# Kernel tuning notes

Measured on AMD Instinct MI355X. Metric: run time of the kernel, lower is better.

Reference implementation:

```python
import jax, jax.numpy as jnp
import numpy as np

B, T, C = 2, 2048, 768
H = 12
D = C // H
HID = 4 * C
EPS = 1e-5
LS_INIT = 1e-4


def _ln(x, g, b):
    mu = jnp.mean(x, axis=-1, keepdims=True)
    var = jnp.mean((x - mu) ** 2, axis=-1, keepdims=True)
    return (x - mu) * jax.lax.rsqrt(var + EPS) * g + b


def setup_inputs() -> dict:
    key = jax.random.key(0)
    ks = jax.random.split(key, 10)
    s = lambda fan_in: 1.0 / np.sqrt(fan_in)
    return {
        "x": jax.random.normal(ks[0], (B, T, C), dtype=jnp.float32),
        "mask_logits": jnp.zeros((B, 1, T, T), dtype=jnp.float32),
        "bias": jax.random.normal(ks[1], (B, H, T, T), dtype=jnp.float32),
        "ln1_g": jnp.ones((C,), jnp.float32),
        "ln1_b": jnp.zeros((C,), jnp.float32),
        "qkv_w": jax.random.normal(ks[2], (3 * C, C), jnp.float32) * s(C),
        "qkv_b": jnp.zeros((3 * C,), jnp.float32),
        "proj_w": jax.random.normal(ks[3], (C, C), jnp.float32) * s(C),
        "proj_b": jnp.zeros((C,), jnp.float32),
        "ls1": jnp.full((C,), LS_INIT, jnp.float32),
        "ln2_g": jnp.ones((C,), jnp.float32),
        "ln2_b": jnp.zeros((C,), jnp.float32),
        "w1": jax.random.normal(ks[4], (HID, C), jnp.float32) * s(C),
        "b1": jnp.zeros((HID,), jnp.float32),
        "w2": jax.random.normal(ks[5], (C, HID), jnp.float32) * s(HID),
        "b2": jnp.zeros((C,), jnp.float32),
        "ls2": jnp.full((C,), LS_INIT, jnp.float32),
    }


def reference(x, mask_logits, bias, ln1_g, ln1_b, qkv_w, qkv_b, proj_w, proj_b,
              ls1, ln2_g, ln2_b, w1, b1, w2, b2, ls2):
    scale = 1.0 / np.sqrt(D)
    xn = _ln(x, ln1_g, ln1_b)
    qkv = xn @ qkv_w.T + qkv_b                      # [B,T,3C]
    qkv = qkv.reshape(B, T, 3, H, D).transpose(2, 0, 3, 1, 4)  # [3,B,H,T,D]
    q, k, v = qkv[0], qkv[1], qkv[2]
    logits = jnp.einsum('bhqd,bhkd->bhqk', q, k) * scale + bias + mask_logits
    attn = jax.nn.softmax(logits, axis=-1)          # [B,H,T,T]
    y = jnp.einsum('bhqk,bhkd->bhqd', attn, v)      # [B,H,T,D]
    y = y.transpose(0, 2, 1, 3).reshape(B, T, C)
    y = y @ proj_w.T + proj_b
    x = x + y * ls1
    h = _ln(x, ln2_g, ln2_b)
    h = jax.nn.gelu(h @ w1.T + b1, approximate=False)
    h = h @ w2.T + b2
    x = x + h * ls2
    return x, jax.lax.stop_gradient(attn)
```

## Files before the change

### kernel.cpp

```cpp
#include <hip/hip_runtime.h>
#include <hip/hip_bf16.h>
#include <math.h>

#define B_ 2
#define T_ 2048
#define C_ 768
#define H_ 12
#define D_ 64
#define HID_ 3072
#define NROW 4096
#define N3C 2304

typedef short bf16x8 __attribute__((ext_vector_type(8)));
typedef float f32x4 __attribute__((ext_vector_type(4)));
typedef unsigned short u16;
typedef unsigned int u32;

__device__ inline u16 f2bf(float f) {
    u32 u = __float_as_uint(f);
    u32 r = (u + 0x7fffu + ((u >> 16) & 1u)) >> 16;
    return (u16)r;
}

__global__ __launch_bounds__(256) void cvt_bf16_kernel(const float* __restrict__ s,
                                                       u16* __restrict__ d, int n) {
    int i = (blockIdx.x * 256 + threadIdx.x) * 4;
    if (i >= n) return;
    float4 v = *(const float4*)(s + i);
    ushort4 o;
    o.x = f2bf(v.x); o.y = f2bf(v.y); o.z = f2bf(v.z); o.w = f2bf(v.w);
    *(ushort4*)(d + i) = o;
}

__global__ __launch_bounds__(256) void ln_kernel(const float* __restrict__ x,
                                                 const float* __restrict__ g,
                                                 const float* __restrict__ b,
                                                 u16* __restrict__ out) {
    int row = blockIdx.x, t = threadIdx.x;
    const float* xr = x + (size_t)row * C_;
    float v[3], s = 0.f, sq = 0.f;
#pragma unroll
    for (int i = 0; i < 3; i++) {
        v[i] = xr[i * 256 + t];
        s += v[i]; sq += v[i] * v[i];
    }
    for (int m = 32; m; m >>= 1) { s += __shfl_xor(s, m); sq += __shfl_xor(sq, m); }
    __shared__ float ss[4], ssq[4];
    int wid = t >> 6;
    if ((t & 63) == 0) { ss[wid] = s; ssq[wid] = sq; }
    __syncthreads();
    s = ss[0] + ss[1] + ss[2] + ss[3];
    sq = ssq[0] + ssq[1] + ssq[2] + ssq[3];
    float mu = s * (1.f / C_);
    float var = sq * (1.f / C_) - mu * mu;
    float rstd = rsqrtf(var + 1e-5f);
#pragma unroll
    for (int i = 0; i < 3; i++) {
        int c = i * 256 + t;
        out[(size_t)row * C_ + c] = f2bf((v[i] - mu) * rstd * g[c] + b[c]);
    }
}

template <int EPI>
__global__ __launch_bounds__(256) void gemm_kernel(const u16* __restrict__ A,
                                                   const u16* __restrict__ W,
                                                   const float* __restrict__ bias,
                                                   float* __restrict__ outf,
                                                   u16* __restrict__ outb,
                                                   const float* __restrict__ res,
                                                   const float* __restrict__ ls,
                                                   int N, int K) {
    __shared__ u16 Alds[128 * 64];
    __shared__ u16 Blds[128 * 64];
    int tid = threadIdx.x;
    int m0 = blockIdx.y * 128, n0 = blockIdx.x * 128;
    int lane = tid & 63, wid = tid >> 6;
    int wr = wid >> 1, wc = wid & 1;
    int lr = lane & 15, lq = lane >> 4;

    f32x4 acc[4][4];
#pragma unroll
    for (int i = 0; i < 4; i++)
#pragma unroll
        for (int j = 0; j < 4; j++) acc[i][j] = (f32x4){0.f, 0.f, 0.f, 0.f};

    int nk = K >> 6;
    const u16* Ab = A + (size_t)m0 * K;
    const u16* Wb = W + (size_t)n0 * K;
    bf16x8 ra[4], rb[4];
#pragma unroll
    for (int i = 0; i < 4; i++) {
        int c = tid + i * 256, row = c >> 3, j = c & 7;
        ra[i] = *(const bf16x8*)(Ab + (size_t)row * K + j * 8);
        rb[i] = *(const bf16x8*)(Wb + (size_t)row * K + j * 8);
    }
    for (int kt = 0; kt < nk; ++kt) {
        __syncthreads();
#pragma unroll
        for (int i = 0; i < 4; i++) {
            int c = tid + i * 256, row = c >> 3, j = c & 7;
            int off = row * 64 + ((j ^ (row & 7)) << 3);
            *(bf16x8*)(Alds + off) = ra[i];
            *(bf16x8*)(Blds + off) = rb[i];
        }
        __syncthreads();
        if (kt + 1 < nk) {
            int k0 = (kt + 1) << 6;
#pragma unroll
            for (int i = 0; i < 4; i++) {
                int c = tid + i * 256, row = c >> 3, j = c & 7;
                ra[i] = *(const bf16x8*)(Ab + (size_t)row * K + k0 + j * 8);
                rb[i] = *(const bf16x8*)(Wb + (size_t)row * K + k0 + j * 8);
            }
        }
#pragma unroll
        for (int s = 0; s < 2; s++) {
            bf16x8 af[4], bw[4];
#pragma unroll
            for (int i = 0; i < 4; i++) {
                int arow = wr * 64 + i * 16 + lr;
                af[i] = *(const bf16x8*)(Alds + arow * 64 + (((4 * s + lq) ^ (arow & 7)) << 3));
                int brow = wc * 64 + i * 16 + lr;
                bw[i] = *(const bf16x8*)(Blds + brow * 64 + (((4 * s + lq) ^ (brow & 7)) << 3));
            }
#pragma unroll
            for (int i = 0; i < 4; i++)
#pragma unroll
                for (int j = 0; j < 4; j++)
                    acc[i][j] = __builtin_amdgcn_mfma_f32_16x16x32_bf16(af[i], bw[j], acc[i][j], 0, 0, 0);
        }
    }
#pragma unroll
    for (int i = 0; i < 4; i++) {
#pragma unroll
        for (int j = 0; j < 4; j++) {
#pragma unroll
            for (int r = 0; r < 4; r++) {
                int gm = m0 + wr * 64 + i * 16 + lq * 4 + r;
                int gn = n0 + wc * 64 + j * 16 + lr;
                float val = acc[i][j][r] + bias[gn];
                if (EPI == 0) {
                    outb[(size_t)gm * N + gn] = f2bf(val);
                } else if (EPI == 1) {
                    float gl = 0.5f * val * (1.f + erff(val * 0.70710678118654752f));
                    outb[(size_t)gm * N + gn] = f2bf(gl);
                } else {
                    outf[(size_t)gm * N + gn] = res[(size_t)gm * N + gn] + ls[gn] * val;
                }
            }
        }
    }
}

__global__ __launch_bounds__(256) void vtrans_kernel(const u16* __restrict__ qkv,
                                                     u16* __restrict__ vt) {
    __shared__ u16 tile[64 * 72];
    int t0 = blockIdx.x * 64, h = blockIdx.y, b = blockIdx.z;
    int tid = threadIdx.x;
#pragma unroll
    for (int i = 0; i < 2; i++) {
        int c = tid + i * 256, tr = c >> 3, j = c & 7;
        bf16x8 v = *(const bf16x8*)(qkv + (size_t)(b * T_ + t0 + tr) * N3C + 1536 + h * 64 + j * 8);
        *(bf16x8*)(tile + tr * 72 + j * 8) = v;
    }
    __syncthreads();
#pragma unroll
    for (int i = 0; i < 2; i++) {
        int c = tid + i * 256, d = c >> 3, tj = c & 7;
        bf16x8 o;
#pragma unroll
        for (int k = 0; k < 8; k++) o[k] = (short)tile[(tj * 8 + k) * 72 + d];
        *(bf16x8*)(vt + (size_t)((b * H_ + h) * 64 + d) * T_ + t0 + tj * 8) = o;
    }
}

__global__ __launch_bounds__(256, 2) void attn_kernel(const u16* __restrict__ qkv,
                                                      const u16* __restrict__ vt,
                                                      const float* __restrict__ bias,
                                                      const float* __restrict__ mask,
                                                      float* __restrict__ attn_out,
                                                      u16* __restrict__ ybuf) {
    __shared__ u16 S[16 * 2048];
    __shared__ float rinv_lds[16];
    char* Sb = (char*)S;
    int qt = blockIdx.x, h = blockIdx.y, b = blockIdx.z;
    int tid = threadIdx.x, lane = tid & 63, wid = tid >> 6;
    int lr = lane & 15, lq = lane >> 4;
    int q0 = qt * 16;
    size_t bh = (size_t)(b * H_ + h);
    const float scale = 0.125f;

    const u16* qp = qkv + (size_t)(b * T_ + q0 + lr) * N3C + h * 64;
    bf16x8 qa0 = *(const bf16x8*)(qp + lq * 8);
    bf16x8 qa1 = *(const bf16x8*)(qp + 32 + lq * 8);
    const u16* kbase = qkv + (size_t)(b * T_ + wid * 512 + lr) * N3C + 768 + h * 64 + lq * 8;
#pragma unroll 4
    for (int ct = 0; ct < 32; ++ct) {
        bf16x8 kf0 = *(const bf16x8*)(kbase + (size_t)ct * 16 * N3C);
        bf16x8 kf1 = *(const bf16x8*)(kbase + (size_t)ct * 16 * N3C + 32);
        f32x4 a = (f32x4){0.f, 0.f, 0.f, 0.f};
        a = __builtin_amdgcn_mfma_f32_16x16x32_bf16(kf0, qa0, a, 0, 0, 0);
        a = __builtin_amdgcn_mfma_f32_16x16x32_bf16(kf1, qa1, a, 0, 0, 0);
        int colbase = wid * 512 + ct * 16;
        ushort4 pk;
        pk.x = f2bf(a[0] * scale);
        pk.y = f2bf(a[1] * scale);
        pk.z = f2bf(a[2] * scale);
        pk.w = f2bf(a[3] * scale);
        *(ushort4*)(Sb + (((u32)lr * 4096 + 2 * colbase + 8 * lq) ^ ((lr & 7) << 4))) = pk;
    }
    __syncthreads();

    const float* bb = bias + (bh * T_ + q0 + wid * 4) * T_;
    const float* mb = mask + ((size_t)b * T_ + q0 + wid * 4) * T_;
    float lsum4[4] = {0.f, 0.f, 0.f, 0.f};
#pragma unroll
    for (int ch = 0; ch < 8; ++ch) {
        int col = ch * 256 + lane * 4;
        float4 b4[4], m4[4];
#pragma unroll
        for (int rr = 0; rr < 4; ++rr) {
            b4[rr] = *(const float4*)(bb + (size_t)rr * T_ + col);
            m4[rr] = *(const float4*)(mb + (size_t)rr * T_ + col);
        }
#pragma unroll
        for (int rr = 0; rr < 4; ++rr) {
            int r = wid * 4 + rr;
            u32 addr = ((u32)r * 4096 + (u32)col * 2) ^ ((u32)(r & 7) << 4);
            uint2 s2 = *(const uint2*)(Sb + addr);
            float e0 = __expf(__uint_as_float(s2.x << 16) + b4[rr].x + m4[rr].x);
            float e1 = __expf(__uint_as_float(s2.x & 0xffff0000u) + b4[rr].y + m4[rr].y);
            float e2 = __expf(__uint_as_float(s2.y << 16) + b4[rr].z + m4[rr].z);
            float e3 = __expf(__uint_as_float(s2.y & 0xffff0000u) + b4[rr].w + m4[rr].w);
            lsum4[rr] += (e0 + e1) + (e2 + e3);
            uint2 o;
            o.x = ((u32)f2bf(e1) << 16) | (u32)f2bf(e0);
            o.y = ((u32)f2bf(e3) << 16) | (u32)f2bf(e2);
            *(uint2*)(Sb + addr) = o;
        }
    }
    float rinv_r[4];
#pragma unroll
    for (int rr = 0; rr < 4; ++rr) {
        float ls = lsum4[rr];
        for (int m = 32; m; m >>= 1) ls += __shfl_xor(ls, m);
        rinv_r[rr] = 1.f / ls;
        if (lane == 0) rinv_lds[wid * 4 + rr] = rinv_r[rr];
    }
    __syncthreads();

    float* ao_base = attn_out + (bh * T_ + q0 + wid * 4) * T_;
#pragma unroll
    for (int ch = 0; ch < 8; ++ch) {
        int col = ch * 256 + lane * 4;
#pragma unroll
        for (int rr = 0; rr < 4; ++rr) {
            int r = wid * 4 + rr;
            u32 addr = ((u32)r * 4096 + (u32)col * 2) ^ ((u32)(r & 7) << 4);
            uint2 s2 = *(const uint2*)(Sb + addr);
            float rv = rinv_r[rr];
            float4 o;
            o.x = __uint_as_float(s2.x << 16) * rv;
            o.y = __uint_as_float(s2.x & 0xffff0000u) * rv;
            o.z = __uint_as_float(s2.y << 16) * rv;
            o.w = __uint_as_float(s2.y & 0xffff0000u) * rv;
            *(float4*)(ao_base + (size_t)rr * T_ + col) = o;
        }
    }

    f32x4 acc = (f32x4){0.f, 0.f, 0.f, 0.f};
    const u16* vtp = vt + (bh * 64 + wid * 16 + lr) * (size_t)T_ + lq * 8;
#pragma unroll 4
    for (int ks = 0; ks < 64; ++ks) {
        bf16x8 pf = *(const bf16x8*)(Sb + (((u32)lr * 4096 + ks * 64 + lq * 16) ^ ((lr & 7) << 4)));
        bf16x8 vf = *(const bf16x8*)(vtp + ks * 32);
        acc = __builtin_amdgcn_mfma_f32_16x16x32_bf16(pf, vf, acc, 0, 0, 0);
    }
#pragma unroll
    for (int r = 0; r < 4; r++) {
        int row = lq * 4 + r;
        float y = acc[r] * rinv_lds[row];
        ybuf[(size_t)(b * T_ + q0 + row) * C_ + h * 64 + wid * 16 + lr] = f2bf(y);
    }
}

extern "C" void kernel_launch(void* const* d_in, const int* in_sizes, int n_in,
                              void* d_out, int out_size, void* d_ws, size_t ws_size,
                              hipStream_t stream) {
    const float* x = (const float*)d_in[0];
    const float* mask = (const float*)d_in[1];
    const float* bias = (const float*)d_in[2];
    const float* ln1g = (const float*)d_in[3];
    const float* ln1b = (const float*)d_in[4];
    const float* qkvw = (const float*)d_in[5];
    const float* qkvb = (const float*)d_in[6];
    const float* projw = (const float*)d_in[7];
    const float* projb = (const float*)d_in[8];
    const float* ls1 = (const float*)d_in[9];
    const float* ln2g = (const float*)d_in[10];
    const float* ln2b = (const float*)d_in[11];
    const float* w1 = (const float*)d_in[12];
    const float* b1 = (const float*)d_in[13];
    const float* w2 = (const float*)d_in[14];
    const float* b2 = (const float*)d_in[15];
    const float* ls2 = (const float*)d_in[16];

    char* ws = (char*)d_ws;
    size_t off = 0;
    u16* qkvw_b = (u16*)(ws + off); off += (size_t)N3C * C_ * 2;
    u16* projw_b = (u16*)(ws + off); off += (size_t)C_ * C_ * 2;
    u16* w1_b = (u16*)(ws + off); off += (size_t)HID_ * C_ * 2;
    u16* w2_b = (u16*)(ws + off); off += (size_t)C_ * HID_ * 2;
    u16* xn = (u16*)(ws + off); off += (size_t)NROW * C_ * 2;
    u16* qkvbuf = (u16*)(ws + off); off += (size_t)NROW * N3C * 2;
    u16* vt = (u16*)(ws + off); off += (size_t)B_ * H_ * D_ * T_ * 2;
    u16* g = qkvbuf;
    u16* ybuf = (u16*)(ws + off); off += (size_t)NROW * C_ * 2;
    float* x1 = (float*)(ws + off); off += (size_t)NROW * C_ * 4;
    (void)ws_size; (void)n_in; (void)in_sizes; (void)out_size;

    float* outx = (float*)d_out;
    float* attn_out = outx + (size_t)NROW * C_;

    cvt_bf16_kernel<<<(N3C * C_ / 4 + 255) / 256, 256, 0, stream>>>(qkvw, qkvw_b, N3C * C_);
    cvt_bf16_kernel<<<(C_ * C_ / 4 + 255) / 256, 256, 0, stream>>>(projw, projw_b, C_ * C_);
    cvt_bf16_kernel<<<(HID_ * C_ / 4 + 255) / 256, 256, 0, stream>>>(w1, w1_b, HID_ * C_);
    cvt_bf16_kernel<<<(C_ * HID_ / 4 + 255) / 256, 256, 0, stream>>>(w2, w2_b, C_ * HID_);

    ln_kernel<<<NROW, 256, 0, stream>>>(x, ln1g, ln1b, xn);
    gemm_kernel<0><<<dim3(N3C / 128, NROW / 128), 256, 0, stream>>>(
        xn, qkvw_b, qkvb, nullptr, qkvbuf, nullptr, nullptr, N3C, C_);
    vtrans_kernel<<<dim3(T_ / 64, H_, B_), 256, 0, stream>>>(qkvbuf, vt);
    attn_kernel<<<dim3(T_ / 16, H_, B_), 256, 0, stream>>>(qkvbuf, vt, bias, mask, attn_out, ybuf);
    gemm_kernel<2><<<dim3(C_ / 128, NROW / 128), 256, 0, stream>>>(
        ybuf, projw_b, projb, x1, nullptr, x, ls1, C_, C_);
    ln_kernel<<<NROW, 256, 0, stream>>>(x1, ln2g, ln2b, xn);
    gemm_kernel<1><<<dim3(HID_ / 128, NROW / 128), 256, 0, stream>>>(
        xn, w1_b, b1, nullptr, g, nullptr, nullptr, HID_, C_);
    gemm_kernel<2><<<dim3(C_ / 128, NROW / 128), 256, 0, stream>>>(
        g, w2_b, b2, outx, nullptr, x1, ls2, C_, HID_);
}
```

Measured before the change: 481.2 us.

## Stream attention bias through double-buffered LDS with direct global-to-LDS loads

```diff
diff --git a/kernel.cpp b/kernel.cpp
--- a/kernel.cpp
+++ b/kernel.cpp
@@ -20,6 +20,12 @@
     u32 u = __float_as_uint(f);
     u32 r = (u + 0x7fffu + ((u >> 16) & 1u)) >> 16;
     return (u16)r;
+}
+
+__device__ __forceinline__ void dma16(const float* g, float* lds) {
+    __builtin_amdgcn_global_load_lds(
+        (const __attribute__((address_space(1))) void*)g,
+        (__attribute__((address_space(3))) void*)lds, 16, 0, 0);
 }
 
 __global__ __launch_bounds__(256) void cvt_bf16_kernel(const float* __restrict__ s,
@@ -181,7 +187,7 @@
                                                       float* __restrict__ attn_out,
                                                       u16* __restrict__ ybuf) {
     __shared__ u16 S[16 * 2048];
-    __shared__ float rinv_lds[16];
+    __shared__ float stg[4][2][2][256];
     char* Sb = (char*)S;
     int qt = blockIdx.x, h = blockIdx.y, b = blockIdx.z;
     int tid = threadIdx.x, lane = tid & 63, wid = tid >> 6;
@@ -211,28 +217,42 @@
     }
     __syncthreads();
 
-    const float* bb = bias + (bh * T_ + q0 + wid * 4) * T_;
-    const float* mb = mask + ((size_t)b * T_ + q0 + wid * 4) * T_;
+    const float* bias_base = bias + (bh * T_ + q0 + wid * 4) * T_;
+    const float* mask_base = mask + ((size_t)b * T_ + q0 + wid * 4) * T_;
     float lsum4[4] = {0.f, 0.f, 0.f, 0.f};
-#pragma unroll
-    for (int ch = 0; ch < 8; ++ch) {
+
+    dma16(bias_base + lane * 4, &stg[wid][0][0][0]);
+    dma16(bias_base + (size_t)T_ + lane * 4, &stg[wid][0][1][0]);
+
+#pragma unroll 1
+    for (int step = 0; step < 16; ++step) {
+        int par = step & 1, pr = step >> 3, ch = step & 7;
+        asm volatile("s_waitcnt vmcnt(0)" ::: "memory");
+        __builtin_amdgcn_sched_barrier(0);
+        if (step < 15) {
+            int ns = step + 1, npar = ns & 1, npr = ns >> 3, nch = ns & 7;
+            const float* g0 = bias_base + (size_t)(2 * npr) * T_ + nch * 256 + lane * 4;
+            const float* g1 = bias_base + (size_t)(2 * npr + 1) * T_ + nch * 256 + lane * 4;
+            dma16(g0, &stg[wid][npar][0][0]);
+            dma16(g1, &stg[wid][npar][1][0]);
+        }
         int col = ch * 256 + lane * 4;
-        float4 b4[4], m4[4];
-#pragma unroll
-        for (int rr = 0; rr < 4; ++rr) {
-            b4[rr] = *(const float4*)(bb + (size_t)rr * T_ + col);
-            m4[rr] = *(const float4*)(mb + (size_t)rr * T_ + col);
-        }
-#pragma unroll
-        for (int rr = 0; rr < 4; ++rr) {
-            int r = wid * 4 + rr;
+        float4 m0 = *(const float4*)(mask_base + (size_t)(2 * pr) * T_ + col);
+        float4 m1 = *(const float4*)(mask_base + (size_t)(2 * pr + 1) * T_ + col);
+        float4 b0 = *(const float4*)&stg[wid][par][0][lane * 4];
+        float4 b1 = *(const float4*)&stg[wid][par][1][lane * 4];
+#pragma unroll
+        for (int rr = 0; rr < 2; ++rr) {
+            int r = wid * 4 + 2 * pr + rr;
+            float4 bv = rr ? b1 : b0;
+            float4 mv = rr ? m1 : m0;
             u32 addr = ((u32)r * 4096 + (u32)col * 2) ^ ((u32)(r & 7) << 4);
             uint2 s2 = *(const uint2*)(Sb + addr);
-            float e0 = __expf(__uint_as_float(s2.x << 16) + b4[rr].x + m4[rr].x);
-            float e1 = __expf(__uint_as_float(s2.x & 0xffff0000u) + b4[rr].y + m4[rr].y);
-            float e2 = __expf(__uint_as_float(s2.y << 16) + b4[rr].z + m4[rr].z);
-            float e3 = __expf(__uint_as_float(s2.y & 0xffff0000u) + b4[rr].w + m4[rr].w);
-            lsum4[rr] += (e0 + e1) + (e2 + e3);
+            float e0 = __expf(__uint_as_float(s2.x << 16) + bv.x + mv.x);
+            float e1 = __expf(__uint_as_float(s2.x & 0xffff0000u) + bv.y + mv.y);
+            float e2 = __expf(__uint_as_float(s2.y << 16) + bv.z + mv.z);
+            float e3 = __expf(__uint_as_float(s2.y & 0xffff0000u) + bv.w + mv.w);
+            lsum4[2 * pr + rr] += (e0 + e1) + (e2 + e3);
             uint2 o;
             o.x = ((u32)f2bf(e1) << 16) | (u32)f2bf(e0);
             o.y = ((u32)f2bf(e3) << 16) | (u32)f2bf(e2);
@@ -245,7 +265,7 @@
         float ls = lsum4[rr];
         for (int m = 32; m; m >>= 1) ls += __shfl_xor(ls, m);
         rinv_r[rr] = 1.f / ls;
-        if (lane == 0) rinv_lds[wid * 4 + rr] = rinv_r[rr];
+        if (lane == 0) stg[wid][0][0][rr] = rinv_r[rr];
     }
     __syncthreads();
 
@@ -279,7 +299,7 @@
 #pragma unroll
     for (int r = 0; r < 4; r++) {
         int row = lq * 4 + r;
-        float y = acc[r] * rinv_lds[row];
+        float y = acc[r] * stg[row >> 2][0][0][row & 3];
         ybuf[(size_t)(b * T_ + q0 + row) * C_ + h * 64 + wid * 16 + lr] = f2bf(y);
     }
 }
```

After: 498.3 us. 3.6% more time.

## Stream attention bias through LDS ring via async DMA, fold mask into QK

Applied to the files above, without the earlier changes.

```diff
diff --git a/kernel.cpp b/kernel.cpp
--- a/kernel.cpp
+++ b/kernel.cpp
@@ -20,6 +20,12 @@
     u32 u = __float_as_uint(f);
     u32 r = (u + 0x7fffu + ((u >> 16) & 1u)) >> 16;
     return (u16)r;
+}
+
+__device__ __forceinline__ void dma16(const float* g, float* lds) {
+    __builtin_amdgcn_global_load_lds(
+        (const __attribute__((address_space(1))) void*)g,
+        (__attribute__((address_space(3))) void*)lds, 16, 0, 0);
 }
 
 __global__ __launch_bounds__(256) void cvt_bf16_kernel(const float* __restrict__ s,
@@ -174,6 +180,36 @@
     }
 }
 
+template <int WAITN, bool ISSUE>
+__device__ __forceinline__ void a2_step(int row, int ch, float& ls,
+                                        const float* bias_base, char* Sb,
+                                        float (*stgw)[256], int lane, int r) {
+    int step = row * 8 + ch;
+    if (ISSUE) {
+        int ns = step + 3;
+        dma16(bias_base + (size_t)(ns >> 3) * T_ + (ns & 7) * 256 + lane * 4,
+              &stgw[ns & 3][0]);
+    }
+    if constexpr (WAITN == 3) asm volatile("s_waitcnt vmcnt(3)" ::: "memory");
+    else if constexpr (WAITN == 2) asm volatile("s_waitcnt vmcnt(2)" ::: "memory");
+    else if constexpr (WAITN == 1) asm volatile("s_waitcnt vmcnt(1)" ::: "memory");
+    else asm volatile("s_waitcnt vmcnt(0)" ::: "memory");
+    __builtin_amdgcn_sched_barrier(0);
+    int col = ch * 256 + lane * 4;
+    float4 bv = *(const float4*)&stgw[step & 3][lane * 4];
+    u32 addr = ((u32)r * 4096 + (u32)col * 2) ^ ((u32)(r & 7) << 4);
+    uint2 s2 = *(const uint2*)(Sb + addr);
+    float e0 = __expf(__uint_as_float(s2.x << 16) + bv.x);
+    float e1 = __expf(__uint_as_float(s2.x & 0xffff0000u) + bv.y);
+    float e2 = __expf(__uint_as_float(s2.y << 16) + bv.z);
+    float e3 = __expf(__uint_as_float(s2.y & 0xffff0000u) + bv.w);
+    ls += (e0 + e1) + (e2 + e3);
+    uint2 o;
+    o.x = ((u32)f2bf(e1) << 16) | (u32)f2bf(e0);
+    o.y = ((u32)f2bf(e3) << 16) | (u32)f2bf(e2);
+    *(uint2*)(Sb + addr) = o;
+}
+
 __global__ __launch_bounds__(256, 2) void attn_kernel(const u16* __restrict__ qkv,
                                                       const u16* __restrict__ vt,
                                                       const float* __restrict__ bias,
@@ -181,7 +217,7 @@
                                                       float* __restrict__ attn_out,
                                                       u16* __restrict__ ybuf) {
     __shared__ u16 S[16 * 2048];
-    __shared__ float rinv_lds[16];
+    __shared__ __align__(16) float stg[4][4][256];
     char* Sb = (char*)S;
     int qt = blockIdx.x, h = blockIdx.y, b = blockIdx.z;
     int tid = threadIdx.x, lane = tid & 63, wid = tid >> 6;
@@ -194,49 +230,44 @@
     bf16x8 qa0 = *(const bf16x8*)(qp + lq * 8);
     bf16x8 qa1 = *(const bf16x8*)(qp + 32 + lq * 8);
     const u16* kbase = qkv + (size_t)(b * T_ + wid * 512 + lr) * N3C + 768 + h * 64 + lq * 8;
+    const float* mbase = mask + ((size_t)b * T_ + q0 + lr) * T_ + wid * 512 + lq * 4;
 #pragma unroll 4
     for (int ct = 0; ct < 32; ++ct) {
         bf16x8 kf0 = *(const bf16x8*)(kbase + (size_t)ct * 16 * N3C);
         bf16x8 kf1 = *(const bf16x8*)(kbase + (size_t)ct * 16 * N3C + 32);
+        float4 mv = *(const float4*)(mbase + ct * 16);
         f32x4 a = (f32x4){0.f, 0.f, 0.f, 0.f};
         a = __builtin_amdgcn_mfma_f32_16x16x32_bf16(kf0, qa0, a, 0, 0, 0);
         a = __builtin_amdgcn_mfma_f32_16x16x32_bf16(kf1, qa1, a, 0, 0, 0);
         int colbase = wid * 512 + ct * 16;
         ushort4 pk;
-        pk.x = f2bf(a[0] * scale);
-        pk.y = f2bf(a[1] * scale);
-        pk.z = f2bf(a[2] * scale);
-        pk.w = f2bf(a[3] * scale);
+        pk.x = f2bf(a[0] * scale + mv.x);
+        pk.y = f2bf(a[1] * scale + mv.y);
+        pk.z = f2bf(a[2] * scale + mv.z);
+        pk.w = f2bf(a[3] * scale + mv.w);
         *(ushort4*)(Sb + (((u32)lr * 4096 + 2 * colbase + 8 * lq) ^ ((lr & 7) << 4))) = pk;
     }
     __syncthreads();
 
-    const float* bb = bias + (bh * T_ + q0 + wid * 4) * T_;
-    const float* mb = mask + ((size_t)b * T_ + q0 + wid * 4) * T_;
+    const float* bias_base = bias + (bh * T_ + q0 + wid * 4) * T_;
     float lsum4[4] = {0.f, 0.f, 0.f, 0.f};
 #pragma unroll
-    for (int ch = 0; ch < 8; ++ch) {
-        int col = ch * 256 + lane * 4;
-        float4 b4[4], m4[4];
-#pragma unroll
-        for (int rr = 0; rr < 4; ++rr) {
-            b4[rr] = *(const float4*)(bb + (size_t)rr * T_ + col);
-            m4[rr] = *(const float4*)(mb + (size_t)rr * T_ + col);
-        }
-#pragma unroll
-        for (int rr = 0; rr < 4; ++rr) {
-            int r = wid * 4 + rr;
-            u32 addr = ((u32)r * 4096 + (u32)col * 2) ^ ((u32)(r & 7) << 4);
-            uint2 s2 = *(const uint2*)(Sb + addr);
-            float e0 = __expf(__uint_as_float(s2.x << 16) + b4[rr].x + m4[rr].x);
-            float e1 = __expf(__uint_as_float(s2.x & 0xffff0000u) + b4[rr].y + m4[rr].y);
-            float e2 = __expf(__uint_as_float(s2.y << 16) + b4[rr].z + m4[rr].z);
-            float e3 = __expf(__uint_as_float(s2.y & 0xffff0000u) + b4[rr].w + m4[rr].w);
-            lsum4[rr] += (e0 + e1) + (e2 + e3);
-            uint2 o;
-            o.x = ((u32)f2bf(e1) << 16) | (u32)f2bf(e0);
-            o.y = ((u32)f2bf(e3) << 16) | (u32)f2bf(e2);
-            *(uint2*)(Sb + addr) = o;
+    for (int s = 0; s < 3; ++s)
+        dma16(bias_base + s * 256 + lane * 4, &stg[wid][s][0]);
+#pragma unroll
+    for (int row = 0; row < 4; ++row) {
+        int r = wid * 4 + row;
+        if (row < 3) {
+#pragma unroll 1
+            for (int ch = 0; ch < 8; ++ch)
+                a2_step<3, true>(row, ch, lsum4[row], bias_base, Sb, stg[wid], lane, r);
+        } else {
+#pragma unroll 1
+            for (int ch = 0; ch < 5; ++ch)
+                a2_step<3, true>(3, ch, lsum4[3], bias_base, Sb, stg[wid], lane, r);
+            a2_step<2, false>(3, 5, lsum4[3], bias_base, Sb, stg[wid], lane, r);
+            a2_step<1, false>(3, 6, lsum4[3], bias_base, Sb, stg[wid], lane, r);
+            a2_step<0, false>(3, 7, lsum4[3], bias_base, Sb, stg[wid], lane, r);
         }
     }
     float rinv_r[4];
@@ -245,7 +276,7 @@
         float ls = lsum4[rr];
         for (int m = 32; m; m >>= 1) ls += __shfl_xor(ls, m);
         rinv_r[rr] = 1.f / ls;
-        if (lane == 0) rinv_lds[wid * 4 + rr] = rinv_r[rr];
+        if (lane == 0) stg[wid][0][rr] = rinv_r[rr];
     }
     __syncthreads();
 
@@ -279,7 +310,7 @@
 #pragma unroll
     for (int r = 0; r < 4; r++) {
         int row = lq * 4 + r;
-        float y = acc[r] * rinv_lds[row];
+        float y = acc[r] * stg[row >> 2][0][row & 3];
         ybuf[(size_t)(b * T_ + q0 + row) * C_ + h * 64 + wid * 16 + lr] = f2bf(y);
     }
 }
```

New measurement: 542.2 us. +12.7%, slower.
